# Kernel tuning notes

Measured on AMD Instinct MI355X. Metric: run time of the kernel, lower is better.

Reference implementation:

```python
import jax, jax.numpy as jnp
import numpy as np

D_MODEL = 2048
N_HEADS = 16
N_KV = 4
GROUP = N_HEADS // N_KV  # 4
D_K = D_MODEL // N_HEADS  # 128
D_V = D_MODEL // N_KV     # 512
THETA = 10000.0
Q_DIM = N_HEADS * D_K
K_DIM = N_KV * D_K
V_DIM = N_KV * D_V


def _apply_rope(t, sin, cos):
    # t: [B, H, L, D]; sin/cos: [L, D] broadcast over batch/heads
    half = t.shape[-1] // 2
    x1, x2 = t[..., :half], t[..., half:]
    rot = jnp.concatenate([-x2, x1], axis=-1)
    return t * cos + rot * sin


def setup_inputs() -> dict:
    key = jax.random.key(0)
    k1, k2, k3 = jax.random.split(key, 3)
    x = jax.random.normal(k1, (2, 2048, D_MODEL), dtype=jnp.float32)
    # attn_proj: Linear(d_model -> Q_DIM+K_DIM+V_DIM, bias=False); stored as [in, out]
    W_attn = jax.random.normal(k2, (D_MODEL, Q_DIM + K_DIM + V_DIM), dtype=jnp.float32) * 0.02
    # out_proj: Linear(n_heads*d_v -> d_model) with bias
    W_out = jax.random.normal(k3, (N_HEADS * D_V, D_MODEL), dtype=jnp.float32) * 0.02
    b_out = jnp.zeros((D_MODEL,), dtype=jnp.float32)
    return {"x": x, "W_attn": W_attn, "W_out": W_out, "b_out": b_out}


def reference(x, W_attn, W_out, b_out):
    B, L, _ = x.shape
    qkv = x @ W_attn  # [B, L, Q_DIM+K_DIM+V_DIM]
    q = qkv[..., :Q_DIM].reshape(B, L, N_HEADS, D_K).transpose(0, 2, 1, 3)          # [B,H,L,dk]
    k = qkv[..., Q_DIM:Q_DIM + K_DIM].reshape(B, L, N_KV, D_K).transpose(0, 2, 1, 3)  # [B,Hkv,L,dk]
    v = qkv[..., Q_DIM + K_DIM:].reshape(B, L, N_KV, D_V).transpose(0, 2, 1, 3)       # [B,Hkv,L,dv]

    # RoPE (computed in float32, as in source)
    inv_freq = 1.0 / (THETA ** (jnp.arange(0, D_K, 2, dtype=jnp.float32) / D_K))
    freqs = jnp.arange(L, dtype=jnp.float32)[:, None] * inv_freq[None, :]  # [L, dk/2]
    ang = jnp.concatenate([freqs, freqs], axis=-1)                          # [L, dk]
    sin, cos = jnp.sin(ang), jnp.cos(ang)
    q = _apply_rope(q.astype(jnp.float32), sin, cos).astype(x.dtype)
    k = _apply_rope(k.astype(jnp.float32), sin, cos).astype(x.dtype)

    # GQA: repeat_interleave(group, dim=1) is equivalent to grouping q heads as [kv, group]
    qg = q.reshape(B, N_KV, GROUP, L, D_K)
    scores = jnp.einsum('bkgqd,bkld->bkgql', qg, k) / (D_K ** 0.5)  # [B,Hkv,G,L,L]
    probs = jax.nn.softmax(scores, axis=-1)
    ctx = jnp.einsum('bkgql,bkle->bkgqe', probs, v)  # [B,Hkv,G,L,dv]
    ctx = ctx.reshape(B, N_HEADS, L, D_V).transpose(0, 2, 1, 3).reshape(B, L, N_HEADS * D_V)
    return ctx @ W_out + b_out
```

## Files before the change

### kernel.cpp

```cpp
#include <hip/hip_runtime.h>

typedef unsigned short u16;
typedef float f32x4 __attribute__((ext_vector_type(4)));
typedef __bf16 bf16x8 __attribute__((ext_vector_type(8)));

#define DEV static __device__ __forceinline__

DEV u16 f2bf(float f) {
  union { float f; unsigned u; } c; c.f = f;
  unsigned u = c.u;
  u += 0x7fffu + ((u >> 16) & 1u);
  return (u16)(u >> 16);
}
DEV float bf2f(u16 h) {
  union { float f; unsigned u; } c; c.u = ((unsigned)h) << 16;
  return c.f;
}
DEV f32x4 MFMA(bf16x8 a, bf16x8 b, f32x4 c) {
  return __builtin_amdgcn_mfma_f32_16x16x32_bf16(a, b, c, 0, 0, 0);
}
DEV unsigned cvt_pk_bf16(float a, float b) {
  unsigned r;
  asm("v_cvt_pk_bf16_f32 %0, %1, %2" : "=v"(r) : "v"(a), "v"(b));
  return r;
}
DEV float ex2(float x) { return __builtin_amdgcn_exp2f(x); }
DEV void glds16(const void* src, void* lds) {
  __builtin_amdgcn_global_load_lds(
      (__attribute__((address_space(1))) void*)src,
      (__attribute__((address_space(3))) void*)lds, 16, 0, 0);
}


__global__ void rope_tables(float* __restrict__ sinT, float* __restrict__ cosT) {
  int idx = blockIdx.x * 256 + threadIdx.x;
  int l = idx >> 6, i = idx & 63;
  float inv = __expf(-((float)(2 * i) / 128.0f) * 9.210340371976184f);
  float ang = (float)l * inv;
  sinT[idx] = sinf(ang);
  cosT[idx] = cosf(ang);
}

__global__ void cast_f32_bf16(const float* __restrict__ in, u16* __restrict__ out) {
  int i = (blockIdx.x * 256 + threadIdx.x) * 4;
  float4 v = *(const float4*)(in + i);
  ushort4 o;
  o.x = f2bf(v.x); o.y = f2bf(v.y); o.z = f2bf(v.z); o.w = f2bf(v.w);
  *(ushort4*)(out + i) = o;
}

__global__ void transpose_cast(const float* __restrict__ in, u16* __restrict__ out,
                               int R, int C) {
  __shared__ u16 tile[32][33];
  int c0 = blockIdx.x * 32, r0 = blockIdx.y * 32;
  int tx = threadIdx.x, ty = threadIdx.y;
  for (int i = 0; i < 32; i += 8)
    tile[ty + i][tx] = f2bf(in[(size_t)(r0 + ty + i) * C + c0 + tx]);
  __syncthreads();
  for (int i = 0; i < 32; i += 8)
    out[(size_t)(c0 + ty + i) * R + r0 + tx] = tile[tx][ty + i];
}

template <int WRITE_F32>
__global__ __launch_bounds__(256) void gemm_bt(
    const u16* __restrict__ A, const u16* __restrict__ Bt,
    float* __restrict__ Cf, u16* __restrict__ Cb,
    const float* __restrict__ bias, int N, int K) {
  __shared__ __align__(16) u16 lA[128 * 32];
  __shared__ __align__(16) u16 lB[128 * 32];
  const int bn = blockIdx.x, bm = blockIdx.y;
  const int t = threadIdx.x, w = t >> 6, l = t & 63;
  const int wr = w >> 1, wc = w & 1;
  const int lr = l & 15, lg = l >> 4;

  f32x4 zero = {0.f, 0.f, 0.f, 0.f};
  f32x4 acc[4][4];
#pragma unroll
  for (int m = 0; m < 4; ++m)
#pragma unroll
    for (int n = 0; n < 4; ++n) acc[m][n] = zero;

  const int lrow = l >> 2, lslot = l & 3;
  const size_t aBase = (size_t)(bm * 128) * K;
  const size_t bBase = (size_t)(bn * 128) * K;

  for (int k0 = 0; k0 < K; k0 += 32) {
    __syncthreads();
#pragma unroll
    for (int i = 0; i < 2; ++i) {
      int R = w * 16 + i * 64;
      int row = R + lrow;
      int sg = (lslot ^ (row & 3)) * 8;
      glds16(A + aBase + (size_t)row * K + k0 + sg, (u16*)lA + R * 32);
      glds16(Bt + bBase + (size_t)row * K + k0 + sg, (u16*)lB + R * 32);
    }
    __syncthreads();

    bf16x8 af[4], bf[4];
#pragma unroll
    for (int m = 0; m < 4; ++m) {
      int row = wr * 64 + m * 16 + lr;
      int sw = (lg ^ (row & 3)) & 3;
      af[m] = *(const bf16x8*)((char*)lA + row * 64 + sw * 16);
    }
#pragma unroll
    for (int n = 0; n < 4; ++n) {
      int row = wc * 64 + n * 16 + lr;
      int sw = (lg ^ (row & 3)) & 3;
      bf[n] = *(const bf16x8*)((char*)lB + row * 64 + sw * 16);
    }
#pragma unroll
    for (int m = 0; m < 4; ++m)
#pragma unroll
      for (int n = 0; n < 4; ++n)
        acc[m][n] = MFMA(af[m], bf[n], acc[m][n]);
  }

#pragma unroll
  for (int m = 0; m < 4; ++m) {
#pragma unroll
    for (int n = 0; n < 4; ++n) {
      int col = bn * 128 + wc * 64 + n * 16 + lr;
      float bv = WRITE_F32 ? bias[col] : 0.f;
#pragma unroll
      for (int j = 0; j < 4; ++j) {
        size_t rowg = (size_t)(bm * 128 + wr * 64 + m * 16 + lg * 4 + j);
        float v = acc[m][n][j];
        if (WRITE_F32) Cf[rowg * N + col] = v + bv;
        else           Cb[rowg * N + col] = f2bf(v);
      }
    }
  }
}

__global__ void rope_kernel(u16* __restrict__ qkv, const float* __restrict__ sinT,
                            const float* __restrict__ cosT) {
  int idx = blockIdx.x * 256 + threadIdx.x;
  int d = idx & 63;
  int rh = idx >> 6;
  int head = rh % 20;
  int row = rh / 20;
  int lpos = row & 2047;
  int col = head < 16 ? head * 128 : 2048 + (head - 16) * 128;
  float sc = head < 16 ? 0.12751743561938476f : 1.0f;
  u16* p = qkv + (size_t)row * 4608 + col;
  float x1 = bf2f(p[d]), x2 = bf2f(p[d + 64]);
  float c = cosT[lpos * 64 + d], s = sinT[lpos * 64 + d];
  p[d]      = f2bf((x1 * c - x2 * s) * sc);
  p[d + 64] = f2bf((x2 * c + x1 * s) * sc);
}

__global__ void vt_kernel(const u16* __restrict__ qkv, u16* __restrict__ vT) {
  __shared__ u16 tile[32][33];
  int bkv = blockIdx.z;
  int b = bkv >> 2, kv = bkv & 3;
  int e0 = blockIdx.x * 32, l0 = blockIdx.y * 32;
  const u16* src = qkv + (size_t)(b * 2048) * 4608 + 2560 + kv * 512;
  int tx = threadIdx.x, ty = threadIdx.y;
  for (int i = 0; i < 32; i += 8)
    tile[ty + i][tx] = src[(size_t)(l0 + ty + i) * 4608 + e0 + tx];
  __syncthreads();
  u16* dst = vT + (size_t)(bkv * 512) * 2048;
  int pi = ((tx >> 2) & 3) * 8 + ((tx >> 4) & 1) * 4 + (tx & 3);
  for (int i = 0; i < 32; i += 8)
    dst[(size_t)(e0 + ty + i) * 2048 + l0 + pi] = tile[tx][ty + i];
}

__global__ __launch_bounds__(512, 2) void attn_kernel(
    const u16* __restrict__ qkv, const u16* __restrict__ vT,
    u16* __restrict__ ctxb) {
  const int wg = blockIdx.x;
  const int pg = wg & 7, qt = wg >> 3;
  const int kvg = pg & 3, b = pg >> 2;
  const int t = threadIdx.x, w = t >> 6, l = t & 63;
  const int lr = l & 15, lg = l >> 4;
  const int h4 = w >> 1, eh = w & 1;
  const int h = kvg * 4 + h4;

  __shared__ __align__(16) u16 lK[2][32 * 128];
  __shared__ __align__(16) u16 lV[2][256 * 64];

  f32x4 zero = {0.f, 0.f, 0.f, 0.f};

  bf16x8 qf[2][4];
  const size_t qbase = (size_t)(b * 2048 + qt * 32);
#pragma unroll
  for (int m = 0; m < 2; ++m)
#pragma unroll
    for (int dc = 0; dc < 4; ++dc)
      qf[m][dc] = *(const bf16x8*)(qkv + (qbase + m * 16 + lr) * 4608 + h * 128 + dc * 32 + lg * 8);

  f32x4 acc[2][16];
#pragma unroll
  for (int m = 0; m < 2; ++m)
#pragma unroll
    for (int e = 0; e < 16; ++e) acc[m][e] = zero;
  float m_r[2] = {-1e30f, -1e30f};
  float l_r[2] = {0.f, 0.f};

  const size_t kbase = (size_t)(b * 2048) * 4608 + 2048 + kvg * 128;
  const size_t vbase = (size_t)((b * 4 + kvg) * 512) * 2048;

  const int krow = t >> 4;
  const int kp = t & 15;
  const int ks = (kp & 8) | ((kp ^ (krow & 7)) & 7);
  const u16* ksrc0 = qkv + kbase + (size_t)krow * 4608 + ks * 8;
  const int vs = (t & 7) ^ ((t >> 3) & 7);
  const int ve0 = (t >> 3) * 2 + (vs >> 2);
  const u16* vsrc0 = vT + vbase + (size_t)ve0 * 2048 + (vs & 3) * 8;

  const int vfoff = (eh * 128 + (lr >> 1)) * 128 +
                    (((((lr & 1) << 2) | lg) ^ ((lr >> 1) & 7)) << 4);

  auto stage = [&](int bi, int kv0) {
    glds16(ksrc0 + (size_t)kv0 * 4608, &lK[bi][t * 8]);
#pragma unroll
    for (int i = 0; i < 4; ++i)
      glds16(vsrc0 + kv0 + (size_t)i * 262144, &lV[bi][i * 4096 + t * 8]);
  };

  stage(0, 0);

  for (int it = 0; it < 64; ++it) {
    const int cur = it & 1;
    __syncthreads();
    if (it + 1 < 64) stage(cur ^ 1, 32 * (it + 1));
    const char* lKc = (const char*)lK[cur];
    const char* lVc = (const char*)lV[cur];

    f32x4 sT[2][2];
    sT[0][0] = zero; sT[0][1] = zero; sT[1][0] = zero; sT[1][1] = zero;
#pragma unroll
    for (int dc = 0; dc < 4; ++dc) {
      int slot = dc * 4 + lg;
      int sw = (slot & 8) | ((slot ^ (lr & 7)) & 7);
#pragma unroll
      for (int kt = 0; kt < 2; ++kt) {
        bf16x8 kf = *(const bf16x8*)(lKc + (kt * 16 + lr) * 256 + sw * 16);
        sT[kt][0] = MFMA(kf, qf[0][dc], sT[kt][0]);
        sT[kt][1] = MFMA(kf, qf[1][dc], sT[kt][1]);
      }
    }

    float rmax[2];
#pragma unroll
    for (int m = 0; m < 2; ++m) {
      float a0 = fmaxf(fmaxf(sT[0][m][0], sT[0][m][1]), fmaxf(sT[0][m][2], sT[0][m][3]));
      float a1 = fmaxf(fmaxf(sT[1][m][0], sT[1][m][1]), fmaxf(sT[1][m][2], sT[1][m][3]));
      float r = fmaxf(a0, a1);
      r = fmaxf(r, __shfl_xor(r, 16));
      r = fmaxf(r, __shfl_xor(r, 32));
      rmax[m] = r;
    }
    bool need = (rmax[0] > m_r[0] + 11.5f) || (rmax[1] > m_r[1] + 11.5f);
    if (__any(need)) {
#pragma unroll
      for (int m = 0; m < 2; ++m) {
        float mn = fmaxf(m_r[m], rmax[m]);
        float al = ex2(m_r[m] - mn);
        m_r[m] = mn; l_r[m] *= al;
        float alj[4];
#pragma unroll
        for (int j = 0; j < 4; ++j) alj[j] = __shfl(al, lg * 4 + j);
#pragma unroll
        for (int e = 0; e < 16; ++e)
#pragma unroll
          for (int j = 0; j < 4; ++j) acc[m][e][j] *= alj[j];
      }
    }

    bf16x8 pf[2];
#pragma unroll
    for (int m = 0; m < 2; ++m) {
      float p0 = ex2(sT[0][m][0] - m_r[m]), p1 = ex2(sT[0][m][1] - m_r[m]);
      float p2 = ex2(sT[0][m][2] - m_r[m]), p3 = ex2(sT[0][m][3] - m_r[m]);
      float p4 = ex2(sT[1][m][0] - m_r[m]), p5 = ex2(sT[1][m][1] - m_r[m]);
      float p6 = ex2(sT[1][m][2] - m_r[m]), p7 = ex2(sT[1][m][3] - m_r[m]);
      float s = ((p0 + p1) + (p2 + p3)) + ((p4 + p5) + (p6 + p7));
      s += __shfl_xor(s, 16);
      s += __shfl_xor(s, 32);
      l_r[m] += s;
      union { bf16x8 v; unsigned wd[4]; } u;
      u.wd[0] = cvt_pk_bf16(p0, p1);
      u.wd[1] = cvt_pk_bf16(p2, p3);
      u.wd[2] = cvt_pk_bf16(p4, p5);
      u.wd[3] = cvt_pk_bf16(p6, p7);
      pf[m] = u.v;
    }

#pragma unroll
    for (int e = 0; e < 16; ++e) {
      bf16x8 vf = *(const bf16x8*)(lVc + vfoff + e * 1024);
      acc[0][e] = MFMA(pf[0], vf, acc[0][e]);
      acc[1][e] = MFMA(pf[1], vf, acc[1][e]);
    }
  }

#pragma unroll
  for (int m = 0; m < 2; ++m) {
    float linv[4];
#pragma unroll
    for (int j = 0; j < 4; ++j) linv[j] = 1.0f / __shfl(l_r[m], lg * 4 + j);
    const size_t orow0 = qbase + m * 16 + lg * 4;
#pragma unroll
    for (int e = 0; e < 16; ++e)
#pragma unroll
      for (int j = 0; j < 4; ++j)
        ctxb[(orow0 + j) * 8192 + h * 512 + eh * 256 + e * 16 + lr] =
            f2bf(acc[m][e][j] * linv[j]);
  }
}

extern "C" void kernel_launch(void* const* d_in, const int* in_sizes, int n_in,
                              void* d_out, int out_size, void* d_ws, size_t ws_size,
                              hipStream_t stream) {
  const float* x      = (const float*)d_in[0];
  const float* W_attn = (const float*)d_in[1];
  const float* W_out  = (const float*)d_in[2];
  const float* b_out  = (const float*)d_in[3];
  float* out = (float*)d_out;
  char* ws = (char*)d_ws;

  if (ws_size < 158334976u) return;

  float* sinT = (float*)(ws + 0);
  float* cosT = (float*)(ws + 524288);
  u16* xb   = (u16*)(ws + 1048576);
  u16* WbT  = (u16*)(ws + 17825792);
  u16* qkvb = (u16*)(ws + 36700160);
  u16* vT   = (u16*)(ws + 74448896);
  u16* ctxb = (u16*)(ws + 91226112);
  u16* WobT = (u16*)(ws + 1048576);

  rope_tables<<<512, 256, 0, stream>>>(sinT, cosT);
  cast_f32_bf16<<<8192, 256, 0, stream>>>(x, xb);
  transpose_cast<<<dim3(144, 64), dim3(32, 8), 0, stream>>>(W_attn, WbT, 2048, 4608);
  gemm_bt<0><<<dim3(36, 32), 256, 0, stream>>>(xb, WbT, nullptr, qkvb, nullptr, 4608, 2048);
  rope_kernel<<<20480, 256, 0, stream>>>(qkvb, sinT, cosT);
  vt_kernel<<<dim3(16, 64, 8), dim3(32, 8), 0, stream>>>(qkvb, vT);
  attn_kernel<<<512, 512, 0, stream>>>(qkvb, vT, ctxb);
  transpose_cast<<<dim3(64, 256), dim3(32, 8), 0, stream>>>(W_out, WobT, 8192, 2048);
  gemm_bt<1><<<dim3(16, 32), 256, 0, stream>>>(ctxb, WobT, out, nullptr, b_out, 2048, 8192);
}
```

Before: 629.5 us.

## Replace generic GEMM with double-buffered multi-phase pipelined 256-tile GEMMs

Replaces the single-buffered 128x128 GEMM with two specialized 512-thread kernels using 256x256 (QKV projection) and 256x128 (output projection) tiles. Global-to-LDS loads are double-buffered, issued in phases between MFMA batches, and gated by explicit vmcnt waits and raw barriers, with MFMA priority raised. Block indices are swizzled so neighbouring blocks share input tiles in cache. The aim is to hide memory latency and raise data reuse per block. In exchange it uses more LDS and registers, hard-codes the problem shapes, and depends on hand-placed wait counts being correct.

```diff
diff --git a/kernel.cpp b/kernel.cpp
--- a/kernel.cpp
+++ b/kernel.cpp
@@ -30,6 +30,16 @@
       (__attribute__((address_space(1))) void*)src,
       (__attribute__((address_space(3))) void*)lds, 16, 0, 0);
 }
+DEV void barrier_raw() {
+  __builtin_amdgcn_sched_barrier(0);
+  asm volatile("s_barrier" ::: "memory");
+  __builtin_amdgcn_sched_barrier(0);
+}
+#define VMCNT(N)                                              \
+  do {                                                        \
+    asm volatile("s_waitcnt vmcnt(" #N ")" ::: "memory");     \
+    __builtin_amdgcn_sched_barrier(0);                        \
+  } while (0)
 
 
 __global__ void rope_tables(float* __restrict__ sinT, float* __restrict__ cosT) {
@@ -61,75 +71,188 @@
     out[(size_t)(c0 + ty + i) * R + r0 + tx] = tile[tx][ty + i];
 }
 
-template <int WRITE_F32>
-__global__ __launch_bounds__(256) void gemm_bt(
-    const u16* __restrict__ A, const u16* __restrict__ Bt,
-    float* __restrict__ Cf, u16* __restrict__ Cb,
-    const float* __restrict__ bias, int N, int K) {
-  __shared__ __align__(16) u16 lA[128 * 32];
-  __shared__ __align__(16) u16 lB[128 * 32];
-  const int bn = blockIdx.x, bm = blockIdx.y;
+__global__ __launch_bounds__(512) void gemm1_8ph(const u16* __restrict__ A,
+                                                 const u16* __restrict__ Bt,
+                                                 u16* __restrict__ C) {
+  constexpr int K = 2048, N = 4608, NT = 32;
+  __shared__ __align__(16) u16 lA[2][2][8192];
+  __shared__ __align__(16) u16 lB[2][2][8192];
   const int t = threadIdx.x, w = t >> 6, l = t & 63;
-  const int wr = w >> 1, wc = w & 1;
   const int lr = l & 15, lg = l >> 4;
-
-  f32x4 zero = {0.f, 0.f, 0.f, 0.f};
+  const int wr = w >> 2, wn = w & 3;
+  const int swz = (blockIdx.x & 7) * 36 + (blockIdx.x >> 3);
+  const int bm = swz & 15, bn = swz >> 4;
+
+  const size_t aBase = (size_t)(bm * 256) * K;
+  const size_t bBase = (size_t)(bn * 256) * K;
+  const int lslog = (t & 3) ^ ((t >> 3) & 3);
+  const int r128 = t >> 2;
+  const int aswz = (lg ^ ((lr >> 1) & 3)) << 4;
+
+  auto stA = [&](int buf, int kk, int tile) {
+#pragma unroll
+    for (int i = 0; i < 2; ++i) {
+      int row = i * 128 + r128;
+      glds16(A + aBase + (size_t)row * K + tile * 64 + kk * 32 + lslog * 8,
+             &lA[buf][kk][i * 4096 + t * 8]);
+    }
+  };
+  auto stB = [&](int buf, int kk, int tile) {
+#pragma unroll
+    for (int i = 0; i < 2; ++i) {
+      int row = i * 128 + r128;
+      glds16(Bt + bBase + (size_t)row * K + tile * 64 + kk * 32 + lslog * 8,
+             &lB[buf][kk][i * 4096 + t * 8]);
+    }
+  };
+
+  f32x4 acc[8][4];
+#pragma unroll
+  for (int f = 0; f < 8; ++f)
+#pragma unroll
+    for (int g = 0; g < 4; ++g) acc[f][g] = f32x4{0.f, 0.f, 0.f, 0.f};
+
+  stA(0, 0, 0); stB(0, 0, 0); stA(0, 1, 0); stB(0, 1, 0); stA(1, 0, 1); stB(1, 0, 1);
+  VMCNT(8);
+  barrier_raw();
+
+  auto PH = [&](int buf, int kk, int mh, auto&& st) {
+    bf16x8 af[4], bb[4];
+    const char* pA = (const char*)lA[buf][kk];
+    const char* pB = (const char*)lB[buf][kk];
+#pragma unroll
+    for (int f = 0; f < 4; ++f) {
+      af[f] = *(const bf16x8*)(pA + (wr * 128 + (mh * 4 + f) * 16 + lr) * 64 + aswz);
+      bb[f] = *(const bf16x8*)(pB + (wn * 64 + f * 16 + lr) * 64 + aswz);
+    }
+    st();
+    __builtin_amdgcn_s_setprio(1);
+#pragma unroll
+    for (int f = 0; f < 4; ++f)
+#pragma unroll
+      for (int g = 0; g < 4; ++g)
+        acc[mh * 4 + f][g] = MFMA(af[f], bb[g], acc[mh * 4 + f][g]);
+    __builtin_amdgcn_s_setprio(0);
+  };
+  auto NOST = [] {};
+
+  for (int i = 0; i < NT / 2 - 1; ++i) {
+    const int t1 = 2 * i + 1, t2 = 2 * i + 2, t3 = 2 * i + 3;
+    PH(0, 0, 0, [&] { stA(1, 1, t1); });            barrier_raw();
+    PH(0, 0, 1, [&] { stB(1, 1, t1); }); VMCNT(8);  barrier_raw();
+    PH(0, 1, 0, [&] { stA(0, 0, t2); });            barrier_raw();
+    PH(0, 1, 1, [&] { stB(0, 0, t2); }); VMCNT(8);  barrier_raw();
+    PH(1, 0, 0, [&] { stA(0, 1, t2); });            barrier_raw();
+    PH(1, 0, 1, [&] { stB(0, 1, t2); }); VMCNT(8);  barrier_raw();
+    PH(1, 1, 0, [&] { stA(1, 0, t3); });            barrier_raw();
+    PH(1, 1, 1, [&] { stB(1, 0, t3); }); VMCNT(8);  barrier_raw();
+  }
+  PH(0, 0, 0, [&] { stA(1, 1, NT - 1); });           barrier_raw();
+  PH(0, 0, 1, [&] { stB(1, 1, NT - 1); }); VMCNT(8); barrier_raw();
+  PH(0, 1, 0, NOST);                                 barrier_raw();
+  PH(0, 1, 1, NOST);                       VMCNT(4); barrier_raw();
+  PH(1, 0, 0, NOST);                                 barrier_raw();
+  PH(1, 0, 1, NOST);                       VMCNT(0); barrier_raw();
+  PH(1, 1, 0, NOST);                                 barrier_raw();
+  PH(1, 1, 1, NOST);
+
+  const int crow0 = bm * 256 + wr * 128;
+  const int ccol0 = bn * 256 + wn * 64;
+#pragma unroll
+  for (int f = 0; f < 8; ++f)
+#pragma unroll
+    for (int g = 0; g < 4; ++g)
+#pragma unroll
+      for (int j = 0; j < 4; ++j)
+        C[(size_t)(crow0 + f * 16 + lg * 4 + j) * N + ccol0 + g * 16 + lr] =
+            f2bf(acc[f][g][j]);
+}
+
+__global__ __launch_bounds__(512) void gemm2_4ph(const u16* __restrict__ A,
+                                                 const u16* __restrict__ Bt,
+                                                 float* __restrict__ Cf,
+                                                 const float* __restrict__ bias) {
+  constexpr int K = 8192, N = 2048, NT = 128;
+  __shared__ __align__(16) u16 lA[2][2][8192];
+  __shared__ __align__(16) u16 lB[2][2][4096];
+  const int t = threadIdx.x, w = t >> 6, l = t & 63;
+  const int lr = l & 15, lg = l >> 4;
+  const int wr = w >> 1, wn = w & 1;
+  const int swz = (blockIdx.x & 7) * 32 + (blockIdx.x >> 3);
+  const int bm = swz & 15, bn = swz >> 4;
+
+  const size_t aBase = (size_t)(bm * 256) * K;
+  const size_t bBase = (size_t)(bn * 128) * K;
+  const int lslog = (t & 3) ^ ((t >> 3) & 3);
+  const int r128 = t >> 2;
+  const int aswz = (lg ^ ((lr >> 1) & 3)) << 4;
+
+  auto stA = [&](int buf, int kk, int tile) {
+#pragma unroll
+    for (int i = 0; i < 2; ++i) {
+      int row = i * 128 + r128;
+      glds16(A + aBase + (size_t)row * K + tile * 64 + kk * 32 + lslog * 8,
+             &lA[buf][kk][i * 4096 + t * 8]);
+    }
+  };
+  auto stB = [&](int buf, int kk, int tile) {
+    glds16(Bt + bBase + (size_t)r128 * K + tile * 64 + kk * 32 + lslog * 8,
+           &lB[buf][kk][t * 8]);
+  };
+
   f32x4 acc[4][4];
 #pragma unroll
-  for (int m = 0; m < 4; ++m)
-#pragma unroll
-    for (int n = 0; n < 4; ++n) acc[m][n] = zero;
-
-  const int lrow = l >> 2, lslot = l & 3;
-  const size_t aBase = (size_t)(bm * 128) * K;
-  const size_t bBase = (size_t)(bn * 128) * K;
-
-  for (int k0 = 0; k0 < K; k0 += 32) {
-    __syncthreads();
-#pragma unroll
-    for (int i = 0; i < 2; ++i) {
-      int R = w * 16 + i * 64;
-      int row = R + lrow;
-      int sg = (lslot ^ (row & 3)) * 8;
-      glds16(A + aBase + (size_t)row * K + k0 + sg, (u16*)lA + R * 32);
-      glds16(Bt + bBase + (size_t)row * K + k0 + sg, (u16*)lB + R * 32);
-    }
-    __syncthreads();
-
-    bf16x8 af[4], bf[4];
-#pragma unroll
-    for (int m = 0; m < 4; ++m) {
-      int row = wr * 64 + m * 16 + lr;
-      int sw = (lg ^ (row & 3)) & 3;
-      af[m] = *(const bf16x8*)((char*)lA + row * 64 + sw * 16);
-    }
-#pragma unroll
-    for (int n = 0; n < 4; ++n) {
-      int row = wc * 64 + n * 16 + lr;
-      int sw = (lg ^ (row & 3)) & 3;
-      bf[n] = *(const bf16x8*)((char*)lB + row * 64 + sw * 16);
-    }
-#pragma unroll
-    for (int m = 0; m < 4; ++m)
-#pragma unroll
-      for (int n = 0; n < 4; ++n)
-        acc[m][n] = MFMA(af[m], bf[n], acc[m][n]);
+  for (int f = 0; f < 4; ++f)
+#pragma unroll
+    for (int g = 0; g < 4; ++g) acc[f][g] = f32x4{0.f, 0.f, 0.f, 0.f};
+
+  stA(0, 0, 0); stB(0, 0, 0); stA(0, 1, 0); stB(0, 1, 0); stA(1, 0, 1); stB(1, 0, 1);
+  VMCNT(6);
+  barrier_raw();
+
+  auto PH = [&](int buf, int kk, auto&& st) {
+    bf16x8 af[4], bb[4];
+    const char* pA = (const char*)lA[buf][kk];
+    const char* pB = (const char*)lB[buf][kk];
+#pragma unroll
+    for (int f = 0; f < 4; ++f) {
+      af[f] = *(const bf16x8*)(pA + (wr * 64 + f * 16 + lr) * 64 + aswz);
+      bb[f] = *(const bf16x8*)(pB + (wn * 64 + f * 16 + lr) * 64 + aswz);
+    }
+    st();
+    __builtin_amdgcn_s_setprio(1);
+#pragma unroll
+    for (int f = 0; f < 4; ++f)
+#pragma unroll
+      for (int g = 0; g < 4; ++g)
+        acc[f][g] = MFMA(af[f], bb[g], acc[f][g]);
+    __builtin_amdgcn_s_setprio(0);
+  };
+  auto NOST = [] {};
+
+  for (int i = 0; i < NT / 2 - 1; ++i) {
+    const int t1 = 2 * i + 1, t2 = 2 * i + 2, t3 = 2 * i + 3;
+    PH(0, 0, [&] { stA(1, 1, t1); stB(1, 1, t1); }); VMCNT(6); barrier_raw();
+    PH(0, 1, [&] { stA(0, 0, t2); stB(0, 0, t2); }); VMCNT(6); barrier_raw();
+    PH(1, 0, [&] { stA(0, 1, t2); stB(0, 1, t2); }); VMCNT(6); barrier_raw();
+    PH(1, 1, [&] { stA(1, 0, t3); stB(1, 0, t3); }); VMCNT(6); barrier_raw();
   }
-
-#pragma unroll
-  for (int m = 0; m < 4; ++m) {
-#pragma unroll
-    for (int n = 0; n < 4; ++n) {
-      int col = bn * 128 + wc * 64 + n * 16 + lr;
-      float bv = WRITE_F32 ? bias[col] : 0.f;
-#pragma unroll
-      for (int j = 0; j < 4; ++j) {
-        size_t rowg = (size_t)(bm * 128 + wr * 64 + m * 16 + lg * 4 + j);
-        float v = acc[m][n][j];
-        if (WRITE_F32) Cf[rowg * N + col] = v + bv;
-        else           Cb[rowg * N + col] = f2bf(v);
-      }
-    }
+  PH(0, 0, [&] { stA(1, 1, NT - 1); stB(1, 1, NT - 1); }); VMCNT(6); barrier_raw();
+  PH(0, 1, NOST);                                          VMCNT(3); barrier_raw();
+  PH(1, 0, NOST);                                          VMCNT(0); barrier_raw();
+  PH(1, 1, NOST);
+
+  const int crow0 = bm * 256 + wr * 64;
+  const int ccol0 = bn * 128 + wn * 64;
+#pragma unroll
+  for (int g = 0; g < 4; ++g) {
+    float bv = bias[ccol0 + g * 16 + lr];
+#pragma unroll
+    for (int f = 0; f < 4; ++f)
+#pragma unroll
+      for (int j = 0; j < 4; ++j)
+        Cf[(size_t)(crow0 + f * 16 + lg * 4 + j) * N + ccol0 + g * 16 + lr] =
+            acc[f][g][j] + bv;
   }
 }
 
@@ -335,10 +458,10 @@
   rope_tables<<<512, 256, 0, stream>>>(sinT, cosT);
   cast_f32_bf16<<<8192, 256, 0, stream>>>(x, xb);
   transpose_cast<<<dim3(144, 64), dim3(32, 8), 0, stream>>>(W_attn, WbT, 2048, 4608);
-  gemm_bt<0><<<dim3(36, 32), 256, 0, stream>>>(xb, WbT, nullptr, qkvb, nullptr, 4608, 2048);
+  gemm1_8ph<<<288, 512, 0, stream>>>(xb, WbT, qkvb);
   rope_kernel<<<20480, 256, 0, stream>>>(qkvb, sinT, cosT);
   vt_kernel<<<dim3(16, 64, 8), dim3(32, 8), 0, stream>>>(qkvb, vT);
   attn_kernel<<<512, 512, 0, stream>>>(qkvb, vT, ctxb);
   transpose_cast<<<dim3(64, 256), dim3(32, 8), 0, stream>>>(W_out, WobT, 8192, 2048);
-  gemm_bt<1><<<dim3(16, 32), 256, 0, stream>>>(ctxb, WobT, out, nullptr, b_out, 2048, 8192);
-}
+  gemm2_4ph<<<256, 512, 0, stream>>>(ctxb, WobT, out, b_out);
+}
```

Result: faster. 571.6 us (-9.2%).
